# Optimization experiments

Measured on AMD Instinct MI355X. Metric: run time of the kernel, lower is better.

Reference implementation:

```python
import jax, jax.numpy as jnp
import numpy as np

BLOCK_SIZE = 32
NUM_PROJS = 7


def _unit_hamming(n):
    # AngularLSH._unit_hamming_distance_array (Gray-code-like permutation)
    a = np.array([0, 1], dtype=np.int32)
    for i in range(1, n):
        a = np.concatenate([a, a[::-1] + 2 ** i])
    return a


def _lsh_hash(x, proj_dir, perm, enc_vec):
    # x: [B,H,N,D], proj_dir: [1,1,D,P] -> hash ids [B,H,N]
    pd = proj_dir[0, 0]  # [D,P]
    proj = jnp.einsum('bhnd,dp->bhnp', x, pd)
    bits = (proj > 0).astype(jnp.int32)
    bin_ids = (bits * enc_vec).sum(-1)
    return perm[bin_ids]


def _causal_attn(q, k, v):
    # q,k,v: [B,N,H,D] (xformers layout), causal softmax attention
    B, N, H, D = q.shape
    s = jnp.einsum('bqhd,bkhd->bhqk', q, k) * (D ** -0.5)
    causal = jnp.tril(jnp.ones((N, N), dtype=bool))
    s = jnp.where(causal, s, jnp.finfo(s.dtype).min)
    w = jax.nn.softmax(s, axis=-1)
    return jnp.einsum('bhqk,bkhd->bqhd', w, v)


def _forward(q, k, v, proj_dir):
    B, N, H, D = q.shape
    bs = BLOCK_SIZE
    nb = N // bs
    perm = jnp.asarray(_unit_hamming(NUM_PROJS))
    enc_vec = jnp.asarray(2 ** np.arange(NUM_PROJS, dtype=np.int32))

    qt = jnp.transpose(q, (0, 2, 1, 3))  # [B,H,N,D]
    kt = jnp.transpose(k, (0, 2, 1, 3))

    q_hash = _lsh_hash(qt, proj_dir, perm, enc_vec)  # [B,H,N]
    sort_idx = jnp.argsort(q_hash, axis=2, stable=True)
    q_hash_sort = jnp.take_along_axis(q_hash, sort_idx, axis=2)
    inv_idx = jnp.argsort(sort_idx, axis=2, stable=True)
    q_sorted = jnp.take_along_axis(qt, sort_idx[..., None], axis=2)  # [B,H,N,D]

    k_hash = _lsh_hash(kt, proj_dir, perm, enc_vec)  # [B,H,N]

    # torch .view(seq_len, -1) on [B,H,N] contiguous tensors (C-order reshape)
    qh_rows = q_hash_sort.reshape(N, -1)  # [N, B*H]
    kh_rows = k_hash.reshape(N, -1)
    eq = (qh_rows == kh_rows).reshape(nb, -1)  # rows grouped by query block
    keep = (eq.sum(axis=1) > 0)  # [nb] block kept if any hash match

    # K_split_per_block = k.reshape(B, nb, -1, D) on [B,H,N,D]
    k_blocks = kt.reshape(B, nb, (H * N) // nb, D)
    k_blocks = k_blocks * keep[None, :, None, None].astype(kt.dtype)
    k_crit = k_blocks.reshape(B, H, N, D)

    # out_critical = attn(q_critical, k_critical, v_critical) then unsort
    out = _causal_attn(jnp.transpose(q_sorted, (0, 2, 1, 3)),
                       jnp.transpose(k_crit, (0, 2, 1, 3)),
                       v)  # [B,N,H,D]
    out = jnp.take_along_axis(jnp.transpose(out, (0, 2, 1, 3)), inv_idx[..., None], axis=2)
    return jnp.transpose(out, (0, 2, 1, 3))  # [B,N,H,D]


def setup_inputs() -> dict:
    key = jax.random.key(0)
    k1, k2, k3, k4 = jax.random.split(key, 4)
    B, N, H, D = 2, 2048, 16, 128
    return {
        'q': jax.random.normal(k1, (B, N, H, D), dtype=jnp.float32),
        'k': jax.random.normal(k2, (B, N, H, D), dtype=jnp.float32),
        'v': jax.random.normal(k3, (B, N, H, D), dtype=jnp.float32),
        'proj_dir': jax.random.normal(k4, (1, 1, D, NUM_PROJS), dtype=jnp.float32),
        'is_causal': 1,
        'mask': jnp.zeros((1, 1), dtype=bool),
    }


def reference(q, k, v, proj_dir, is_causal, mask):
    # is_causal is always True at every attention call site; mask is unused then.
    return _forward(q, k, v, proj_dir)
```

## Files before the change

### kernel.cpp

```cpp
#include <hip/hip_runtime.h>
#include <cstdint>

#define BB 2
#define NN 2048
#define HH 16
#define DD 128
#define BH 32
#define NPROJ 7

typedef __bf16 bf16x8 __attribute__((ext_vector_type(8)));
typedef float f32x4 __attribute__((ext_vector_type(4)));

__device__ __forceinline__ unsigned short f2bf(float f) {
  unsigned int u = __float_as_uint(f);
  u += 0x7fff + ((u >> 16) & 1);
  return (unsigned short)(u >> 16);
}

__device__ __forceinline__ bf16x8 load_q8(const float* p) {
  float4 a = *(const float4*)p;
  float4 b = *(const float4*)(p + 4);
  unsigned short r[8] = {f2bf(a.x), f2bf(a.y), f2bf(a.z), f2bf(a.w),
                         f2bf(b.x), f2bf(b.y), f2bf(b.z), f2bf(b.w)};
  return *(bf16x8*)r;
}

__global__ void prep_kernel(const float* __restrict__ q, const float* __restrict__ k,
                            const float* __restrict__ v, const float* __restrict__ pd,
                            int* __restrict__ qh, int* __restrict__ kh,
                            unsigned short* __restrict__ Vt, unsigned short* __restrict__ Kb) {
  __shared__ __align__(16) char smem[64 * 132 * 2];
  if (blockIdx.x < 4096) {
    float* spd = (float*)smem;
    for (int i = threadIdx.x; i < DD * NPROJ; i += 256) spd[i] = pd[i];
    __syncthreads();
    long long gid = (long long)blockIdx.x * 256 + threadIdx.x;
    int part = (int)(gid & 7);
    long long row = gid >> 3;
    const long long NR = (long long)BB * NN * HH;
    int isk = row >= NR;
    long long r = isk ? row - NR : row;
    const float* src = (isk ? k : q) + r * DD + part * 16;
    double acc[NPROJ];
    for (int p = 0; p < NPROJ; ++p) acc[p] = 0.0;
    __align__(16) unsigned short kb16[16];
    for (int d = 0; d < 16; d += 4) {
      float4 x = *(const float4*)(src + d);
      if (isk) {
        kb16[d + 0] = f2bf(x.x); kb16[d + 1] = f2bf(x.y);
        kb16[d + 2] = f2bf(x.z); kb16[d + 3] = f2bf(x.w);
      }
      int dbase = part * 16 + d;
      for (int p = 0; p < NPROJ; ++p) {
        acc[p] += (double)x.x * (double)spd[(dbase + 0) * NPROJ + p]
                + (double)x.y * (double)spd[(dbase + 1) * NPROJ + p]
                + (double)x.z * (double)spd[(dbase + 2) * NPROJ + p]
                + (double)x.w * (double)spd[(dbase + 3) * NPROJ + p];
      }
    }
    int b_ = (int)(r / (NN * HH));
    int rem = (int)(r % (NN * HH));
    int n_ = rem / HH, h_ = rem % HH;
    if (isk) {
      unsigned short* dst = Kb + (((long long)(b_ * HH + h_) * NN + n_) << 7) + part * 16;
      *(uint4*)dst = *(const uint4*)&kb16[0];
      *(uint4*)(dst + 8) = *(const uint4*)&kb16[8];
    }
    for (int off = 1; off < 8; off <<= 1)
      for (int p = 0; p < NPROJ; ++p) acc[p] += __shfl_xor(acc[p], off);
    if (part == 0) {
      int bin = 0;
      for (int p = 0; p < NPROJ; ++p) bin |= ((int)(acc[p] > 0.0)) << p;
      int hsh = bin ^ (bin >> 1);
      (isk ? kh : qh)[((long long)b_ * HH + h_) * NN + n_] = hsh;
    }
  } else {
    unsigned short (*tile)[132] = (unsigned short(*)[132])smem;
    int blk = blockIdx.x - 4096;
    int bh = blk >> 5;
    int n0 = (blk & 31) * 64;
    int b = bh >> 4, h = bh & 15;
    for (int it = 0; it < 8; ++it) {
      int cid = it * 256 + threadIdx.x;
      int r = cid >> 5, d4 = (cid & 31) * 4;
      float4 x = *(const float4*)(v + (((long long)(b * NN + n0 + r) * HH + h) << 7) + d4);
      *(ushort4*)&tile[r][d4] = make_ushort4(f2bf(x.x), f2bf(x.y), f2bf(x.z), f2bf(x.w));
    }
    __syncthreads();
    for (int it = 0; it < 8; ++it) {
      int cid = it * 256 + threadIdx.x;
      int d = cid >> 4, n4 = (cid & 15) * 4;
      ushort4 y = make_ushort4(tile[n4 + 0][d], tile[n4 + 1][d], tile[n4 + 2][d], tile[n4 + 3][d]);
      *(ushort4*)(Vt + ((long long)bh * DD + d) * NN + n0 + n4) = y;
    }
  }
}

__global__ void sortkeep_kernel(const int* __restrict__ qh, const int* __restrict__ kh,
                                int* __restrict__ sidx, int* __restrict__ keep) {
  __shared__ int sh[NN];
  __shared__ int cnt[4][128];
  __shared__ int cum[128];
  __shared__ int kflag[2];
  int bh = blockIdx.x;
  const int* src = qh + (long long)bh * NN;
  for (int i = threadIdx.x; i < NN; i += 512) sh[i] = src[i];
  if (threadIdx.x < 2) kflag[threadIdx.x] = 0;
  __syncthreads();
  int bin = threadIdx.x & 127, seg = threadIdx.x >> 7;
  int n0 = seg * (NN / 4);
  int c = 0;
  for (int n = n0; n < n0 + NN / 4; ++n) c += (sh[n] == bin);
  cnt[seg][bin] = c;
  __syncthreads();
  if (threadIdx.x == 0) {
    int run = 0;
    for (int t = 0; t < 128; ++t) {
      cum[t] = run;
      run += cnt[0][t] + cnt[1][t] + cnt[2][t] + cnt[3][t];
    }
  }
  __syncthreads();
  int pos = cum[bin];
  for (int s = 0; s < seg; ++s) pos += cnt[s][bin];
  int f0 = 0, f1 = 0;
  for (int n = n0; n < n0 + NN / 4; ++n)
    if (sh[n] == bin) {
      sidx[(long long)bh * NN + pos] = n;
      int match = (bin == kh[(long long)bh * NN + pos]);
      if (pos < 1024) f0 |= match; else f1 |= match;
      ++pos;
    }
  if (f0) atomicOr(&kflag[0], 1);
  if (f1) atomicOr(&kflag[1], 1);
  __syncthreads();
  if (threadIdx.x < 2) keep[bh * 2 + threadIdx.x] = kflag[threadIdx.x];
}

__global__ __launch_bounds__(256, 2)
void flash_kernel(const float* __restrict__ q, const unsigned short* __restrict__ Kb,
                  const unsigned short* __restrict__ Vt, const int* __restrict__ sidx,
                  const int* __restrict__ keep, float* __restrict__ out) {
  __shared__ __align__(16) unsigned short Kt[2][64 * 136];
  __shared__ __align__(16) unsigned short Vs[2][128 * 72];
  __shared__ __align__(16) unsigned short Pb[4][16 * 72];

  int bx = blockIdx.x;
  int bh = blockIdx.y;
  int b = bh >> 4, h = bh & 15;
  int tid = threadIdx.x;
  int w = tid >> 6, lane = tid & 63;
  int l16 = lane & 15, qd = lane >> 4;

  const unsigned short* Kh = Kb + (long long)bh * NN * DD;
  const unsigned short* Vb = Vt + (long long)bh * DD * NN;
  const float scale = 0.088388347648318447f;

  const int ksr = tid >> 4;
  const int ksc = (tid & 15) * 8;
  const int vsr = tid >> 3;
  const int vsc = (tid & 7) * 8;

  uint4 kreg[4], vreg[4];

#define STAGE_LOAD(K0, KP)                                                            \
  {                                                                                   \
    if (KP) {                                                                         \
      _Pragma("unroll")                                                               \
      for (int it = 0; it < 4; ++it)                                                  \
        kreg[it] = *(const uint4*)(Kh + (long long)((K0) + it * 16 + ksr) * DD + ksc);\
    } else {                                                                          \
      _Pragma("unroll")                                                               \
      for (int it = 0; it < 4; ++it) kreg[it] = make_uint4(0, 0, 0, 0);               \
    }                                                                                 \
    _Pragma("unroll")                                                                 \
    for (int it = 0; it < 4; ++it)                                                    \
      vreg[it] = *(const uint4*)(Vb + (long long)(it * 32 + vsr) * NN + (K0) + vsc);  \
  }

#define STAGE_WRITE(BUF)                                                              \
  {                                                                                   \
    _Pragma("unroll")                                                                 \
    for (int it = 0; it < 4; ++it)                                                    \
      *(uint4*)&Kt[BUF][(it * 16 + ksr) * 136 + ksc] = kreg[it];                      \
    _Pragma("unroll")                                                                 \
    for (int it = 0; it < 4; ++it)                                                    \
      *(uint4*)&Vs[BUF][(it * 32 + vsr) * 72 + vsc] = vreg[it];                       \
  }

  for (int ph = 0; ph < 2; ++ph) {
    int qt = ph ? bx : 31 - bx;
    int qrow = qt * 64 + w * 16 + l16;

    bf16x8 qf[4];
    {
      int nq = sidx[bh * NN + qrow];
      const float* p0 = q + (((long long)(b * NN + nq) * HH + h) << 7) + qd * 8;
#pragma unroll
      for (int c = 0; c < 4; ++c) qf[c] = load_q8(p0 + c * 32);
    }
    f32x4 o[8];
#pragma unroll
    for (int i = 0; i < 8; ++i) o[i] = (f32x4){0.f, 0.f, 0.f, 0.f};
    float m = -__builtin_inff(), l = 0.f;

    int cur = 0;
    STAGE_LOAD(0, keep[h * 4]);
    __syncthreads();
    STAGE_WRITE(0);
    __syncthreads();

    for (int kb = 0; kb <= qt; ++kb) {
      if (kb < qt) STAGE_LOAD((kb + 1) * 64, keep[h * 4 + ((kb + 1) >> 3)]);

      int k0 = kb * 64;
      const unsigned short* Ktc = Kt[cur];
      const unsigned short* Vsc = Vs[cur];

      float s[16];
#pragma unroll
      for (int t = 0; t < 4; ++t) {
        f32x4 a1 = (f32x4){0.f, 0.f, 0.f, 0.f};
#pragma unroll
        for (int c = 0; c < 4; ++c) {
          bf16x8 kf = *(const bf16x8*)&Ktc[(t * 16 + l16) * 136 + c * 32 + qd * 8];
          a1 = __builtin_amdgcn_mfma_f32_16x16x32_bf16(kf, qf[c], a1, 0, 0, 0);
        }
        if (kb == qt) {
#pragma unroll
          for (int r = 0; r < 4; ++r) {
            int keyg = k0 + t * 16 + qd * 4 + r;
            s[t * 4 + r] = (keyg > qrow) ? -__builtin_inff() : a1[r] * scale;
          }
        } else {
#pragma unroll
          for (int r = 0; r < 4; ++r) s[t * 4 + r] = a1[r] * scale;
        }
      }

      {
        float mloc = s[0];
#pragma unroll
        for (int i = 1; i < 16; ++i) mloc = fmaxf(mloc, s[i]);
        mloc = fmaxf(mloc, __shfl_xor(mloc, 16));
        mloc = fmaxf(mloc, __shfl_xor(mloc, 32));
        if (__any(mloc > m)) {
          float mnew = fmaxf(m, mloc);
          float alpha = __expf(m - mnew);
          float aO[4];
#pragma unroll
          for (int r = 0; r < 4; ++r) aO[r] = __shfl(alpha, qd * 4 + r);
#pragma unroll
          for (int c8 = 0; c8 < 8; ++c8)
#pragma unroll
            for (int r = 0; r < 4; ++r) o[c8][r] *= aO[r];
          l *= alpha;
          m = mnew;
        }
        float psum = 0.f;
#pragma unroll
        for (int t = 0; t < 4; ++t) {
          float p0 = __expf(s[t * 4 + 0] - m);
          float p1 = __expf(s[t * 4 + 1] - m);
          float p2 = __expf(s[t * 4 + 2] - m);
          float p3 = __expf(s[t * 4 + 3] - m);
          psum += (p0 + p1) + (p2 + p3);
          *(ushort4*)&Pb[w][l16 * 72 + t * 16 + qd * 4] =
              make_ushort4(f2bf(p0), f2bf(p1), f2bf(p2), f2bf(p3));
        }
        psum += __shfl_xor(psum, 16);
        psum += __shfl_xor(psum, 32);
        l += psum;
      }

#pragma unroll
      for (int g = 0; g < 2; ++g) {
        bf16x8 pf = *(const bf16x8*)&Pb[w][l16 * 72 + g * 32 + qd * 8];
#pragma unroll
        for (int c8 = 0; c8 < 8; ++c8) {
          bf16x8 vf = *(const bf16x8*)&Vsc[(c8 * 16 + l16) * 72 + g * 32 + qd * 8];
          o[c8] = __builtin_amdgcn_mfma_f32_16x16x32_bf16(pf, vf, o[c8], 0, 0, 0);
        }
      }

      if (kb < qt) {
        STAGE_WRITE(cur ^ 1);
        __syncthreads();
        cur ^= 1;
      }
    }

    float lO[4];
    int nO[4];
#pragma unroll
    for (int r = 0; r < 4; ++r) {
      lO[r] = __shfl(l, qd * 4 + r);
      nO[r] = sidx[(long long)bh * NN + qt * 64 + w * 16 + qd * 4 + r];
    }
#pragma unroll
    for (int r = 0; r < 4; ++r) {
      float inv = 1.f / lO[r];
      float* ob = out + (((long long)(b * NN + nO[r]) * HH + h) << 7) + l16;
#pragma unroll
      for (int c8 = 0; c8 < 8; ++c8)
        ob[c8 * 16] = o[c8][r] * inv;
    }
  }
#undef STAGE_LOAD
#undef STAGE_WRITE
}

extern "C" void kernel_launch(void* const* d_in, const int* in_sizes, int n_in,
                              void* d_out, int out_size, void* d_ws, size_t ws_size,
                              hipStream_t stream) {
  const float* q = (const float*)d_in[0];
  const float* k = (const float*)d_in[1];
  const float* v = (const float*)d_in[2];
  const float* pd = (const float*)d_in[3];
  float* out = (float*)d_out;
  char* ws = (char*)d_ws;
  int* qh   = (int*)(ws + 0);
  int* kh   = (int*)(ws + (1u << 18));
  int* sidx = (int*)(ws + (2u << 18));
  int* keep = (int*)(ws + 3u * (1u << 18));
  unsigned short* Vt = (unsigned short*)(ws + (2u << 20));
  unsigned short* Kb = (unsigned short*)(ws + (18u << 20));

  prep_kernel<<<5120, 256, 0, stream>>>(q, k, v, pd, qh, kh, Vt, Kb);
  sortkeep_kernel<<<32, 512, 0, stream>>>(qh, kh, sidx, keep);
  flash_kernel<<<dim3(16, 32), 256, 0, stream>>>(q, Kb, Vt, sidx, keep, out);
}
```

Before: 359.5 us.

## Process two 16-row query groups per wave to double K/V tile reuse

Each wave now computes two 16-row query groups against each staged K/V tile, making the query tile 128 rows per block and halving the grid. This amortizes LDS staging, K fragment loads and V fragment loads over twice the MFMA work. In exchange the kernel holds twice the accumulators and drops to one block per CU, reducing occupancy and latency hiding.

```diff
diff --git a/kernel.cpp b/kernel.cpp
--- a/kernel.cpp
+++ b/kernel.cpp
@@ -137,13 +137,13 @@
   if (threadIdx.x < 2) keep[bh * 2 + threadIdx.x] = kflag[threadIdx.x];
 }
 
-__global__ __launch_bounds__(256, 2)
+__global__ __launch_bounds__(256, 1)
 void flash_kernel(const float* __restrict__ q, const unsigned short* __restrict__ Kb,
                   const unsigned short* __restrict__ Vt, const int* __restrict__ sidx,
                   const int* __restrict__ keep, float* __restrict__ out) {
   __shared__ __align__(16) unsigned short Kt[2][64 * 136];
   __shared__ __align__(16) unsigned short Vs[2][128 * 72];
-  __shared__ __align__(16) unsigned short Pb[4][16 * 72];
+  __shared__ __align__(16) unsigned short Pb[4][32 * 72];
 
   int bx = blockIdx.x;
   int bh = blockIdx.y;
@@ -189,20 +189,32 @@
   }
 
   for (int ph = 0; ph < 2; ++ph) {
-    int qt = ph ? bx : 31 - bx;
-    int qrow = qt * 64 + w * 16 + l16;
-
-    bf16x8 qf[4];
+    int QT = ph ? bx : 15 - bx;
+    int qrowA = QT * 128 + w * 32 + l16;
+    int qrowB = qrowA + 16;
+
+    bf16x8 qfA[4], qfB[4];
     {
-      int nq = sidx[bh * NN + qrow];
-      const float* p0 = q + (((long long)(b * NN + nq) * HH + h) << 7) + qd * 8;
-#pragma unroll
-      for (int c = 0; c < 4; ++c) qf[c] = load_q8(p0 + c * 32);
-    }
-    f32x4 o[8];
-#pragma unroll
-    for (int i = 0; i < 8; ++i) o[i] = (f32x4){0.f, 0.f, 0.f, 0.f};
-    float m = -__builtin_inff(), l = 0.f;
+      int nqA = sidx[bh * NN + qrowA];
+      int nqB = sidx[bh * NN + qrowB];
+      const float* pA = q + (((long long)(b * NN + nqA) * HH + h) << 7) + qd * 8;
+      const float* pB = q + (((long long)(b * NN + nqB) * HH + h) << 7) + qd * 8;
+#pragma unroll
+      for (int c = 0; c < 4; ++c) {
+        qfA[c] = load_q8(pA + c * 32);
+        qfB[c] = load_q8(pB + c * 32);
+      }
+    }
+    f32x4 oA[8], oB[8];
+#pragma unroll
+    for (int i = 0; i < 8; ++i) {
+      oA[i] = (f32x4){0.f, 0.f, 0.f, 0.f};
+      oB[i] = (f32x4){0.f, 0.f, 0.f, 0.f};
+    }
+    float mA = -__builtin_inff(), lA = 0.f;
+    float mB = -__builtin_inff(), lB = 0.f;
+
+    int NKB = 2 * QT + 2;
 
     int cur = 0;
     STAGE_LOAD(0, keep[h * 4]);
@@ -210,100 +222,146 @@
     STAGE_WRITE(0);
     __syncthreads();
 
-    for (int kb = 0; kb <= qt; ++kb) {
-      if (kb < qt) STAGE_LOAD((kb + 1) * 64, keep[h * 4 + ((kb + 1) >> 3)]);
+    for (int kb = 0; kb < NKB; ++kb) {
+      if (kb + 1 < NKB) STAGE_LOAD((kb + 1) * 64, keep[h * 4 + ((kb + 1) >> 3)]);
 
       int k0 = kb * 64;
       const unsigned short* Ktc = Kt[cur];
       const unsigned short* Vsc = Vs[cur];
 
-      float s[16];
+      float sA[16], sB[16];
 #pragma unroll
       for (int t = 0; t < 4; ++t) {
-        f32x4 a1 = (f32x4){0.f, 0.f, 0.f, 0.f};
+        f32x4 aA = (f32x4){0.f, 0.f, 0.f, 0.f};
+        f32x4 aB = (f32x4){0.f, 0.f, 0.f, 0.f};
 #pragma unroll
         for (int c = 0; c < 4; ++c) {
           bf16x8 kf = *(const bf16x8*)&Ktc[(t * 16 + l16) * 136 + c * 32 + qd * 8];
-          a1 = __builtin_amdgcn_mfma_f32_16x16x32_bf16(kf, qf[c], a1, 0, 0, 0);
-        }
-        if (kb == qt) {
+          aA = __builtin_amdgcn_mfma_f32_16x16x32_bf16(kf, qfA[c], aA, 0, 0, 0);
+          aB = __builtin_amdgcn_mfma_f32_16x16x32_bf16(kf, qfB[c], aB, 0, 0, 0);
+        }
+        if (kb >= 2 * QT) {
 #pragma unroll
           for (int r = 0; r < 4; ++r) {
             int keyg = k0 + t * 16 + qd * 4 + r;
-            s[t * 4 + r] = (keyg > qrow) ? -__builtin_inff() : a1[r] * scale;
+            sA[t * 4 + r] = (keyg > qrowA) ? -__builtin_inff() : aA[r] * scale;
+            sB[t * 4 + r] = (keyg > qrowB) ? -__builtin_inff() : aB[r] * scale;
           }
         } else {
 #pragma unroll
-          for (int r = 0; r < 4; ++r) s[t * 4 + r] = a1[r] * scale;
+          for (int r = 0; r < 4; ++r) {
+            sA[t * 4 + r] = aA[r] * scale;
+            sB[t * 4 + r] = aB[r] * scale;
+          }
         }
       }
 
       {
-        float mloc = s[0];
-#pragma unroll
-        for (int i = 1; i < 16; ++i) mloc = fmaxf(mloc, s[i]);
+        float mloc = sA[0];
+#pragma unroll
+        for (int i = 1; i < 16; ++i) mloc = fmaxf(mloc, sA[i]);
         mloc = fmaxf(mloc, __shfl_xor(mloc, 16));
         mloc = fmaxf(mloc, __shfl_xor(mloc, 32));
-        if (__any(mloc > m)) {
-          float mnew = fmaxf(m, mloc);
-          float alpha = __expf(m - mnew);
+        if (__any(mloc > mA)) {
+          float mnew = fmaxf(mA, mloc);
+          float alpha = __expf(mA - mnew);
           float aO[4];
 #pragma unroll
           for (int r = 0; r < 4; ++r) aO[r] = __shfl(alpha, qd * 4 + r);
 #pragma unroll
           for (int c8 = 0; c8 < 8; ++c8)
 #pragma unroll
-            for (int r = 0; r < 4; ++r) o[c8][r] *= aO[r];
-          l *= alpha;
-          m = mnew;
+            for (int r = 0; r < 4; ++r) oA[c8][r] *= aO[r];
+          lA *= alpha;
+          mA = mnew;
         }
         float psum = 0.f;
 #pragma unroll
         for (int t = 0; t < 4; ++t) {
-          float p0 = __expf(s[t * 4 + 0] - m);
-          float p1 = __expf(s[t * 4 + 1] - m);
-          float p2 = __expf(s[t * 4 + 2] - m);
-          float p3 = __expf(s[t * 4 + 3] - m);
+          float p0 = __expf(sA[t * 4 + 0] - mA);
+          float p1 = __expf(sA[t * 4 + 1] - mA);
+          float p2 = __expf(sA[t * 4 + 2] - mA);
+          float p3 = __expf(sA[t * 4 + 3] - mA);
           psum += (p0 + p1) + (p2 + p3);
           *(ushort4*)&Pb[w][l16 * 72 + t * 16 + qd * 4] =
               make_ushort4(f2bf(p0), f2bf(p1), f2bf(p2), f2bf(p3));
         }
         psum += __shfl_xor(psum, 16);
         psum += __shfl_xor(psum, 32);
-        l += psum;
+        lA += psum;
+      }
+      {
+        float mloc = sB[0];
+#pragma unroll
+        for (int i = 1; i < 16; ++i) mloc = fmaxf(mloc, sB[i]);
+        mloc = fmaxf(mloc, __shfl_xor(mloc, 16));
+        mloc = fmaxf(mloc, __shfl_xor(mloc, 32));
+        if (__any(mloc > mB)) {
+          float mnew = fmaxf(mB, mloc);
+          float alpha = __expf(mB - mnew);
+          float aO[4];
+#pragma unroll
+          for (int r = 0; r < 4; ++r) aO[r] = __shfl(alpha, qd * 4 + r);
+#pragma unroll
+          for (int c8 = 0; c8 < 8; ++c8)
+#pragma unroll
+            for (int r = 0; r < 4; ++r) oB[c8][r] *= aO[r];
+          lB *= alpha;
+          mB = mnew;
+        }
+        float psum = 0.f;
+#pragma unroll
+        for (int t = 0; t < 4; ++t) {
+          float p0 = __expf(sB[t * 4 + 0] - mB);
+          float p1 = __expf(sB[t * 4 + 1] - mB);
+          float p2 = __expf(sB[t * 4 + 2] - mB);
+          float p3 = __expf(sB[t * 4 + 3] - mB);
+          psum += (p0 + p1) + (p2 + p3);
+          *(ushort4*)&Pb[w][(16 + l16) * 72 + t * 16 + qd * 4] =
+              make_ushort4(f2bf(p0), f2bf(p1), f2bf(p2), f2bf(p3));
+        }
+        psum += __shfl_xor(psum, 16);
+        psum += __shfl_xor(psum, 32);
+        lB += psum;
       }
 
 #pragma unroll
       for (int g = 0; g < 2; ++g) {
-        bf16x8 pf = *(const bf16x8*)&Pb[w][l16 * 72 + g * 32 + qd * 8];
+        bf16x8 pfA = *(const bf16x8*)&Pb[w][l16 * 72 + g * 32 + qd * 8];
+        bf16x8 pfB = *(const bf16x8*)&Pb[w][(16 + l16) * 72 + g * 32 + qd * 8];
 #pragma unroll
         for (int c8 = 0; c8 < 8; ++c8) {
           bf16x8 vf = *(const bf16x8*)&Vsc[(c8 * 16 + l16) * 72 + g * 32 + qd * 8];
-          o[c8] = __builtin_amdgcn_mfma_f32_16x16x32_bf16(pf, vf, o[c8], 0, 0, 0);
-        }
-      }
-
-      if (kb < qt) {
+          oA[c8] = __builtin_amdgcn_mfma_f32_16x16x32_bf16(pfA, vf, oA[c8], 0, 0, 0);
+          oB[c8] = __builtin_amdgcn_mfma_f32_16x16x32_bf16(pfB, vf, oB[c8], 0, 0, 0);
+        }
+      }
+
+      if (kb + 1 < NKB) {
         STAGE_WRITE(cur ^ 1);
         __syncthreads();
         cur ^= 1;
       }
     }
 
-    float lO[4];
-    int nO[4];
-#pragma unroll
-    for (int r = 0; r < 4; ++r) {
-      lO[r] = __shfl(l, qd * 4 + r);
-      nO[r] = sidx[(long long)bh * NN + qt * 64 + w * 16 + qd * 4 + r];
-    }
-#pragma unroll
-    for (int r = 0; r < 4; ++r) {
-      float inv = 1.f / lO[r];
-      float* ob = out + (((long long)(b * NN + nO[r]) * HH + h) << 7) + l16;
-#pragma unroll
-      for (int c8 = 0; c8 < 8; ++c8)
-        ob[c8 * 16] = o[c8][r] * inv;
+#pragma unroll
+    for (int grp = 0; grp < 2; ++grp) {
+      float lg = grp ? lB : lA;
+      float lO[4];
+      int nO[4];
+#pragma unroll
+      for (int r = 0; r < 4; ++r) {
+        lO[r] = __shfl(lg, qd * 4 + r);
+        nO[r] = sidx[(long long)bh * NN + QT * 128 + w * 32 + grp * 16 + qd * 4 + r];
+      }
+#pragma unroll
+      for (int r = 0; r < 4; ++r) {
+        float inv = 1.f / lO[r];
+        float* ob = out + (((long long)(b * NN + nO[r]) * HH + h) << 7) + l16;
+#pragma unroll
+        for (int c8 = 0; c8 < 8; ++c8)
+          ob[c8 * 16] = (grp ? oB : oA)[c8][r] * inv;
+      }
     }
   }
 #undef STAGE_LOAD
@@ -328,5 +386,5 @@
 
   prep_kernel<<<5120, 256, 0, stream>>>(q, k, v, pd, qh, kh, Vt, Kb);
   sortkeep_kernel<<<32, 512, 0, stream>>>(qh, kh, sidx, keep);
-  flash_kernel<<<dim3(16, 32), 256, 0, stream>>>(q, Kb, Vt, sidx, keep, out);
-}
+  flash_kernel<<<dim3(8, 32), 256, 0, stream>>>(q, Kb, Vt, sidx, keep, out);
+}
```

Result: slower. 371.5 us (+3.3%).

## Software-pipeline QK of next tile with softmax and PV of current tile

Applied to the files above, without the earlier changes.

Restructures the attention inner loop so the QK^T MFMAs for key tile kb+1 are issued between the softmax of tile kb and its PV accumulation, with two score buffers alternated by manual unrolling. Global prefetch now runs two tiles ahead, and LDS staging gets barriers on both sides. The intent is to overlap matrix-core work with the exp/max/shuffle softmax latency. In exchange it holds more registers (two score arrays), which may cut occupancy, and adds an extra barrier per step.

```diff
diff --git a/kernel.cpp b/kernel.cpp
--- a/kernel.cpp
+++ b/kernel.cpp
@@ -188,6 +188,97 @@
       *(uint4*)&Vs[BUF][(it * 32 + vsr) * 72 + vsc] = vreg[it];                       \
   }
 
+#define QK_TILE(T, S)                                                                 \
+  {                                                                                   \
+    const unsigned short* Ktc_ = Kt[(T) & 1];                                         \
+    int k0_ = (T) * 64;                                                               \
+    _Pragma("unroll")                                                                 \
+    for (int t = 0; t < 4; ++t) {                                                     \
+      f32x4 a1 = (f32x4){0.f, 0.f, 0.f, 0.f};                                         \
+      _Pragma("unroll")                                                               \
+      for (int c = 0; c < 4; ++c) {                                                   \
+        bf16x8 kf = *(const bf16x8*)&Ktc_[(t * 16 + l16) * 136 + c * 32 + qd * 8];    \
+        a1 = __builtin_amdgcn_mfma_f32_16x16x32_bf16(kf, qf[c], a1, 0, 0, 0);         \
+      }                                                                               \
+      if ((T) == qt) {                                                                \
+        _Pragma("unroll")                                                             \
+        for (int r = 0; r < 4; ++r) {                                                 \
+          int keyg = k0_ + t * 16 + qd * 4 + r;                                       \
+          (S)[t * 4 + r] = (keyg > qrow) ? -__builtin_inff() : a1[r] * scale;         \
+        }                                                                             \
+      } else {                                                                        \
+        _Pragma("unroll")                                                             \
+        for (int r = 0; r < 4; ++r) (S)[t * 4 + r] = a1[r] * scale;                   \
+      }                                                                               \
+    }                                                                                 \
+  }
+
+#define SOFTMAX_UPDATE(S)                                                             \
+  {                                                                                   \
+    float x0_ = fmaxf(fmaxf((S)[0], (S)[1]), fmaxf((S)[2], (S)[3]));                  \
+    float x1_ = fmaxf(fmaxf((S)[4], (S)[5]), fmaxf((S)[6], (S)[7]));                  \
+    float x2_ = fmaxf(fmaxf((S)[8], (S)[9]), fmaxf((S)[10], (S)[11]));                \
+    float x3_ = fmaxf(fmaxf((S)[12], (S)[13]), fmaxf((S)[14], (S)[15]));              \
+    float mloc = fmaxf(fmaxf(x0_, x1_), fmaxf(x2_, x3_));                             \
+    mloc = fmaxf(mloc, __shfl_xor(mloc, 16));                                         \
+    mloc = fmaxf(mloc, __shfl_xor(mloc, 32));                                         \
+    if (__any(mloc > m)) {                         \
+      float mnew = fmaxf(m, mloc);                                                    \
+      float alpha = __expf(m - mnew);                                                 \
+      float aO[4];                                                                    \
+      _Pragma("unroll")                                                               \
+      for (int r = 0; r < 4; ++r) aO[r] = __shfl(alpha, qd * 4 + r);                  \
+      _Pragma("unroll")                                                               \
+      for (int c8 = 0; c8 < 8; ++c8)                                                  \
+        _Pragma("unroll")                                                             \
+        for (int r = 0; r < 4; ++r) o[c8][r] *= aO[r];                                \
+      l *= alpha;                                                                     \
+      m = mnew;                                                                       \
+    }                                                                                 \
+    float psum = 0.f;                                                                 \
+    _Pragma("unroll")                                                                 \
+    for (int t = 0; t < 4; ++t) {                                                     \
+      float p0 = __expf((S)[t * 4 + 0] - m);                                          \
+      float p1 = __expf((S)[t * 4 + 1] - m);                                          \
+      float p2 = __expf((S)[t * 4 + 2] - m);                                          \
+      float p3 = __expf((S)[t * 4 + 3] - m);                                          \
+      psum += (p0 + p1) + (p2 + p3);                                                  \
+      *(ushort4*)&Pb[w][l16 * 72 + t * 16 + qd * 4] =                                 \
+          make_ushort4(f2bf(p0), f2bf(p1), f2bf(p2), f2bf(p3));                       \
+    }                                                                                 \
+    psum += __shfl_xor(psum, 16);                                                     \
+    psum += __shfl_xor(psum, 32);                                                     \
+    l += psum;                                                                        \
+  }
+
+#define PV_ACC(BUF)                                                                   \
+  {                                                                                   \
+    const unsigned short* Vsc_ = Vs[BUF];                                             \
+    _Pragma("unroll")                                                                 \
+    for (int g = 0; g < 2; ++g) {                                                     \
+      bf16x8 pf = *(const bf16x8*)&Pb[w][l16 * 72 + g * 32 + qd * 8];                 \
+      _Pragma("unroll")                                                               \
+      for (int c8 = 0; c8 < 8; ++c8) {                                                \
+        bf16x8 vf = *(const bf16x8*)&Vsc_[(c8 * 16 + l16) * 72 + g * 32 + qd * 8];    \
+        o[c8] = __builtin_amdgcn_mfma_f32_16x16x32_bf16(pf, vf, o[c8], 0, 0, 0);      \
+      }                                                                               \
+    }                                                                                 \
+  }
+
+#define STEP(KB, SC, SN)                                                              \
+  {                                                                                   \
+    int nxt_ = (KB) + 1;                                                              \
+    if (nxt_ <= qt) {                                                                 \
+      __syncthreads();                       \
+      STAGE_WRITE(nxt_ & 1);                                                          \
+      __syncthreads();                               \
+      if (nxt_ + 1 <= qt) STAGE_LOAD((nxt_ + 1) * 64, keep[h * 4 + ((nxt_ + 1) >> 3)]); \
+    }                                                                                 \
+    SOFTMAX_UPDATE(SC);                                                               \
+    if (nxt_ <= qt) QK_TILE(nxt_, SN);                                                \
+    PV_ACC((KB) & 1);                                                                 \
+  }
+
   for (int ph = 0; ph < 2; ++ph) {
     int qt = ph ? bx : 31 - bx;
     int qrow = qt * 64 + w * 16 + l16;
@@ -204,90 +295,19 @@
     for (int i = 0; i < 8; ++i) o[i] = (f32x4){0.f, 0.f, 0.f, 0.f};
     float m = -__builtin_inff(), l = 0.f;
 
-    int cur = 0;
     STAGE_LOAD(0, keep[h * 4]);
     __syncthreads();
     STAGE_WRITE(0);
     __syncthreads();
-
-    for (int kb = 0; kb <= qt; ++kb) {
-      if (kb < qt) STAGE_LOAD((kb + 1) * 64, keep[h * 4 + ((kb + 1) >> 3)]);
-
-      int k0 = kb * 64;
-      const unsigned short* Ktc = Kt[cur];
-      const unsigned short* Vsc = Vs[cur];
-
-      float s[16];
-#pragma unroll
-      for (int t = 0; t < 4; ++t) {
-        f32x4 a1 = (f32x4){0.f, 0.f, 0.f, 0.f};
-#pragma unroll
-        for (int c = 0; c < 4; ++c) {
-          bf16x8 kf = *(const bf16x8*)&Ktc[(t * 16 + l16) * 136 + c * 32 + qd * 8];
-          a1 = __builtin_amdgcn_mfma_f32_16x16x32_bf16(kf, qf[c], a1, 0, 0, 0);
-        }
-        if (kb == qt) {
-#pragma unroll
-          for (int r = 0; r < 4; ++r) {
-            int keyg = k0 + t * 16 + qd * 4 + r;
-            s[t * 4 + r] = (keyg > qrow) ? -__builtin_inff() : a1[r] * scale;
-          }
-        } else {
-#pragma unroll
-          for (int r = 0; r < 4; ++r) s[t * 4 + r] = a1[r] * scale;
-        }
-      }
-
-      {
-        float mloc = s[0];
-#pragma unroll
-        for (int i = 1; i < 16; ++i) mloc = fmaxf(mloc, s[i]);
-        mloc = fmaxf(mloc, __shfl_xor(mloc, 16));
-        mloc = fmaxf(mloc, __shfl_xor(mloc, 32));
-        if (__any(mloc > m)) {
-          float mnew = fmaxf(m, mloc);
-          float alpha = __expf(m - mnew);
-          float aO[4];
-#pragma unroll
-          for (int r = 0; r < 4; ++r) aO[r] = __shfl(alpha, qd * 4 + r);
-#pragma unroll
-          for (int c8 = 0; c8 < 8; ++c8)
-#pragma unroll
-            for (int r = 0; r < 4; ++r) o[c8][r] *= aO[r];
-          l *= alpha;
-          m = mnew;
-        }
-        float psum = 0.f;
-#pragma unroll
-        for (int t = 0; t < 4; ++t) {
-          float p0 = __expf(s[t * 4 + 0] - m);
-          float p1 = __expf(s[t * 4 + 1] - m);
-          float p2 = __expf(s[t * 4 + 2] - m);
-          float p3 = __expf(s[t * 4 + 3] - m);
-          psum += (p0 + p1) + (p2 + p3);
-          *(ushort4*)&Pb[w][l16 * 72 + t * 16 + qd * 4] =
-              make_ushort4(f2bf(p0), f2bf(p1), f2bf(p2), f2bf(p3));
-        }
-        psum += __shfl_xor(psum, 16);
-        psum += __shfl_xor(psum, 32);
-        l += psum;
-      }
-
-#pragma unroll
-      for (int g = 0; g < 2; ++g) {
-        bf16x8 pf = *(const bf16x8*)&Pb[w][l16 * 72 + g * 32 + qd * 8];
-#pragma unroll
-        for (int c8 = 0; c8 < 8; ++c8) {
-          bf16x8 vf = *(const bf16x8*)&Vsc[(c8 * 16 + l16) * 72 + g * 32 + qd * 8];
-          o[c8] = __builtin_amdgcn_mfma_f32_16x16x32_bf16(pf, vf, o[c8], 0, 0, 0);
-        }
-      }
-
-      if (kb < qt) {
-        STAGE_WRITE(cur ^ 1);
-        __syncthreads();
-        cur ^= 1;
-      }
+    if (qt > 0) STAGE_LOAD(64, keep[h * 4]);
+
+    float s0[16], s1[16];
+    QK_TILE(0, s0);
+
+    int kb = 0;
+    while (true) {
+      STEP(kb, s0, s1); ++kb; if (kb > qt) break;
+      STEP(kb, s1, s0); ++kb; if (kb > qt) break;
     }
 
     float lO[4];
@@ -306,6 +326,10 @@
         ob[c8 * 16] = o[c8][r] * inv;
     }
   }
+#undef STEP
+#undef PV_ACC
+#undef SOFTMAX_UPDATE
+#undef QK_TILE
 #undef STAGE_LOAD
 #undef STAGE_WRITE
 }
```

New measurement: 366.1 us. No clear change (+1.8%).

## Split paired causal query tiles into separate blocks with single-buffered LDS

Applied to the files above, without the earlier changes.

The flash kernel previously paired a heavy and a light causal query tile in each block across 16x32 blocks. It now launches one query tile per block (32x32 grid), ordered longest-first, and drops double-buffered K/V shared memory to a single buffer with an extra barrier, raising the occupancy hint to 3 blocks per SM. It also adds s_setprio around the MFMA sections and uses a tree max reduction. The intent is more parallelism and occupancy, at the cost of less load/compute overlap per block and dependence on the hardware scheduler for balancing the uneven tile lengths.

```diff
diff --git a/kernel.cpp b/kernel.cpp
--- a/kernel.cpp
+++ b/kernel.cpp
@@ -137,16 +137,16 @@
   if (threadIdx.x < 2) keep[bh * 2 + threadIdx.x] = kflag[threadIdx.x];
 }
 
-__global__ __launch_bounds__(256, 2)
+__global__ __launch_bounds__(256, 3)
 void flash_kernel(const float* __restrict__ q, const unsigned short* __restrict__ Kb,
                   const unsigned short* __restrict__ Vt, const int* __restrict__ sidx,
                   const int* __restrict__ keep, float* __restrict__ out) {
-  __shared__ __align__(16) unsigned short Kt[2][64 * 136];
-  __shared__ __align__(16) unsigned short Vs[2][128 * 72];
+  __shared__ __align__(16) unsigned short Kt[64 * 136];
+  __shared__ __align__(16) unsigned short Vs[128 * 72];
   __shared__ __align__(16) unsigned short Pb[4][16 * 72];
 
-  int bx = blockIdx.x;
-  int bh = blockIdx.y;
+  int bh = blockIdx.x;
+  int qt = 31 - (int)blockIdx.y;
   int b = bh >> 4, h = bh & 15;
   int tid = threadIdx.x;
   int w = tid >> 6, lane = tid & 63;
@@ -178,133 +178,132 @@
       vreg[it] = *(const uint4*)(Vb + (long long)(it * 32 + vsr) * NN + (K0) + vsc);  \
   }
 
-#define STAGE_WRITE(BUF)                                                              \
+#define STAGE_WRITE()                                                                 \
   {                                                                                   \
     _Pragma("unroll")                                                                 \
     for (int it = 0; it < 4; ++it)                                                    \
-      *(uint4*)&Kt[BUF][(it * 16 + ksr) * 136 + ksc] = kreg[it];                      \
+      *(uint4*)&Kt[(it * 16 + ksr) * 136 + ksc] = kreg[it];                           \
     _Pragma("unroll")                                                                 \
     for (int it = 0; it < 4; ++it)                                                    \
-      *(uint4*)&Vs[BUF][(it * 32 + vsr) * 72 + vsc] = vreg[it];                       \
-  }
-
-  for (int ph = 0; ph < 2; ++ph) {
-    int qt = ph ? bx : 31 - bx;
-    int qrow = qt * 64 + w * 16 + l16;
-
-    bf16x8 qf[4];
+      *(uint4*)&Vs[(it * 32 + vsr) * 72 + vsc] = vreg[it];                            \
+  }
+
+  int qrow = qt * 64 + w * 16 + l16;
+
+  bf16x8 qf[4];
+  {
+    int nq = sidx[bh * NN + qrow];
+    const float* p0 = q + (((long long)(b * NN + nq) * HH + h) << 7) + qd * 8;
+#pragma unroll
+    for (int c = 0; c < 4; ++c) qf[c] = load_q8(p0 + c * 32);
+  }
+  f32x4 o[8];
+#pragma unroll
+  for (int i = 0; i < 8; ++i) o[i] = (f32x4){0.f, 0.f, 0.f, 0.f};
+  float m = -__builtin_inff(), l = 0.f;
+
+  STAGE_LOAD(0, keep[h * 4]);
+  STAGE_WRITE();
+  __syncthreads();
+
+  for (int kb = 0; kb <= qt; ++kb) {
+    if (kb < qt) STAGE_LOAD((kb + 1) * 64, keep[h * 4 + ((kb + 1) >> 3)]);
+
+    int k0 = kb * 64;
+
+    float s[16];
+    __builtin_amdgcn_s_setprio(1);
+#pragma unroll
+    for (int t = 0; t < 4; ++t) {
+      f32x4 a1 = (f32x4){0.f, 0.f, 0.f, 0.f};
+#pragma unroll
+      for (int c = 0; c < 4; ++c) {
+        bf16x8 kf = *(const bf16x8*)&Kt[(t * 16 + l16) * 136 + c * 32 + qd * 8];
+        a1 = __builtin_amdgcn_mfma_f32_16x16x32_bf16(kf, qf[c], a1, 0, 0, 0);
+      }
+      if (kb == qt) {
+#pragma unroll
+        for (int r = 0; r < 4; ++r) {
+          int keyg = k0 + t * 16 + qd * 4 + r;
+          s[t * 4 + r] = (keyg > qrow) ? -__builtin_inff() : a1[r] * scale;
+        }
+      } else {
+#pragma unroll
+        for (int r = 0; r < 4; ++r) s[t * 4 + r] = a1[r] * scale;
+      }
+    }
+    __builtin_amdgcn_s_setprio(0);
+
     {
-      int nq = sidx[bh * NN + qrow];
-      const float* p0 = q + (((long long)(b * NN + nq) * HH + h) << 7) + qd * 8;
-#pragma unroll
-      for (int c = 0; c < 4; ++c) qf[c] = load_q8(p0 + c * 32);
-    }
-    f32x4 o[8];
-#pragma unroll
-    for (int i = 0; i < 8; ++i) o[i] = (f32x4){0.f, 0.f, 0.f, 0.f};
-    float m = -__builtin_inff(), l = 0.f;
-
-    int cur = 0;
-    STAGE_LOAD(0, keep[h * 4]);
-    __syncthreads();
-    STAGE_WRITE(0);
-    __syncthreads();
-
-    for (int kb = 0; kb <= qt; ++kb) {
-      if (kb < qt) STAGE_LOAD((kb + 1) * 64, keep[h * 4 + ((kb + 1) >> 3)]);
-
-      int k0 = kb * 64;
-      const unsigned short* Ktc = Kt[cur];
-      const unsigned short* Vsc = Vs[cur];
-
-      float s[16];
+      float x0 = fmaxf(fmaxf(s[0], s[1]), fmaxf(s[2], s[3]));
+      float x1 = fmaxf(fmaxf(s[4], s[5]), fmaxf(s[6], s[7]));
+      float x2 = fmaxf(fmaxf(s[8], s[9]), fmaxf(s[10], s[11]));
+      float x3 = fmaxf(fmaxf(s[12], s[13]), fmaxf(s[14], s[15]));
+      float mloc = fmaxf(fmaxf(x0, x1), fmaxf(x2, x3));
+      mloc = fmaxf(mloc, __shfl_xor(mloc, 16));
+      mloc = fmaxf(mloc, __shfl_xor(mloc, 32));
+      if (__any(mloc > m)) {
+        float mnew = fmaxf(m, mloc);
+        float alpha = __expf(m - mnew);
+        float aO[4];
+#pragma unroll
+        for (int r = 0; r < 4; ++r) aO[r] = __shfl(alpha, qd * 4 + r);
+#pragma unroll
+        for (int c8 = 0; c8 < 8; ++c8)
+#pragma unroll
+          for (int r = 0; r < 4; ++r) o[c8][r] *= aO[r];
+        l *= alpha;
+        m = mnew;
+      }
+      float psum = 0.f;
 #pragma unroll
       for (int t = 0; t < 4; ++t) {
-        f32x4 a1 = (f32x4){0.f, 0.f, 0.f, 0.f};
-#pragma unroll
-        for (int c = 0; c < 4; ++c) {
-          bf16x8 kf = *(const bf16x8*)&Ktc[(t * 16 + l16) * 136 + c * 32 + qd * 8];
-          a1 = __builtin_amdgcn_mfma_f32_16x16x32_bf16(kf, qf[c], a1, 0, 0, 0);
-        }
-        if (kb == qt) {
-#pragma unroll
-          for (int r = 0; r < 4; ++r) {
-            int keyg = k0 + t * 16 + qd * 4 + r;
-            s[t * 4 + r] = (keyg > qrow) ? -__builtin_inff() : a1[r] * scale;
-          }
-        } else {
-#pragma unroll
-          for (int r = 0; r < 4; ++r) s[t * 4 + r] = a1[r] * scale;
-        }
-      }
-
-      {
-        float mloc = s[0];
-#pragma unroll
-        for (int i = 1; i < 16; ++i) mloc = fmaxf(mloc, s[i]);
-        mloc = fmaxf(mloc, __shfl_xor(mloc, 16));
-        mloc = fmaxf(mloc, __shfl_xor(mloc, 32));
-        if (__any(mloc > m)) {
-          float mnew = fmaxf(m, mloc);
-          float alpha = __expf(m - mnew);
-          float aO[4];
-#pragma unroll
-          for (int r = 0; r < 4; ++r) aO[r] = __shfl(alpha, qd * 4 + r);
-#pragma unroll
-          for (int c8 = 0; c8 < 8; ++c8)
-#pragma unroll
-            for (int r = 0; r < 4; ++r) o[c8][r] *= aO[r];
-          l *= alpha;
-          m = mnew;
-        }
-        float psum = 0.f;
-#pragma unroll
-        for (int t = 0; t < 4; ++t) {
-          float p0 = __expf(s[t * 4 + 0] - m);
-          float p1 = __expf(s[t * 4 + 1] - m);
-          float p2 = __expf(s[t * 4 + 2] - m);
-          float p3 = __expf(s[t * 4 + 3] - m);
-          psum += (p0 + p1) + (p2 + p3);
-          *(ushort4*)&Pb[w][l16 * 72 + t * 16 + qd * 4] =
-              make_ushort4(f2bf(p0), f2bf(p1), f2bf(p2), f2bf(p3));
-        }
-        psum += __shfl_xor(psum, 16);
-        psum += __shfl_xor(psum, 32);
-        l += psum;
-      }
-
-#pragma unroll
-      for (int g = 0; g < 2; ++g) {
-        bf16x8 pf = *(const bf16x8*)&Pb[w][l16 * 72 + g * 32 + qd * 8];
-#pragma unroll
-        for (int c8 = 0; c8 < 8; ++c8) {
-          bf16x8 vf = *(const bf16x8*)&Vsc[(c8 * 16 + l16) * 72 + g * 32 + qd * 8];
-          o[c8] = __builtin_amdgcn_mfma_f32_16x16x32_bf16(pf, vf, o[c8], 0, 0, 0);
-        }
-      }
-
-      if (kb < qt) {
-        STAGE_WRITE(cur ^ 1);
-        __syncthreads();
-        cur ^= 1;
-      }
-    }
-
-    float lO[4];
-    int nO[4];
-#pragma unroll
-    for (int r = 0; r < 4; ++r) {
-      lO[r] = __shfl(l, qd * 4 + r);
-      nO[r] = sidx[(long long)bh * NN + qt * 64 + w * 16 + qd * 4 + r];
-    }
-#pragma unroll
-    for (int r = 0; r < 4; ++r) {
-      float inv = 1.f / lO[r];
-      float* ob = out + (((long long)(b * NN + nO[r]) * HH + h) << 7) + l16;
-#pragma unroll
-      for (int c8 = 0; c8 < 8; ++c8)
-        ob[c8 * 16] = o[c8][r] * inv;
-    }
+        float p0 = __expf(s[t * 4 + 0] - m);
+        float p1 = __expf(s[t * 4 + 1] - m);
+        float p2 = __expf(s[t * 4 + 2] - m);
+        float p3 = __expf(s[t * 4 + 3] - m);
+        psum += (p0 + p1) + (p2 + p3);
+        *(ushort4*)&Pb[w][l16 * 72 + t * 16 + qd * 4] =
+            make_ushort4(f2bf(p0), f2bf(p1), f2bf(p2), f2bf(p3));
+      }
+      psum += __shfl_xor(psum, 16);
+      psum += __shfl_xor(psum, 32);
+      l += psum;
+    }
+
+    __builtin_amdgcn_s_setprio(1);
+#pragma unroll
+    for (int g = 0; g < 2; ++g) {
+      bf16x8 pf = *(const bf16x8*)&Pb[w][l16 * 72 + g * 32 + qd * 8];
+#pragma unroll
+      for (int c8 = 0; c8 < 8; ++c8) {
+        bf16x8 vf = *(const bf16x8*)&Vs[(c8 * 16 + l16) * 72 + g * 32 + qd * 8];
+        o[c8] = __builtin_amdgcn_mfma_f32_16x16x32_bf16(pf, vf, o[c8], 0, 0, 0);
+      }
+    }
+    __builtin_amdgcn_s_setprio(0);
+
+    if (kb < qt) {
+      __syncthreads();
+      STAGE_WRITE();
+      __syncthreads();
+    }
+  }
+
+  float lO[4];
+  int nO[4];
+#pragma unroll
+  for (int r = 0; r < 4; ++r) {
+    lO[r] = __shfl(l, qd * 4 + r);
+    nO[r] = sidx[(long long)bh * NN + qt * 64 + w * 16 + qd * 4 + r];
+  }
+#pragma unroll
+  for (int r = 0; r < 4; ++r) {
+    float inv = 1.f / lO[r];
+    float* ob = out + (((long long)(b * NN + nO[r]) * HH + h) << 7) + l16;
+#pragma unroll
+    for (int c8 = 0; c8 < 8; ++c8)
+      ob[c8 * 16] = o[c8][r] * inv;
   }
 #undef STAGE_LOAD
 #undef STAGE_WRITE
@@ -328,5 +327,5 @@
 
   prep_kernel<<<5120, 256, 0, stream>>>(q, k, v, pd, qh, kh, Vt, Kb);
   sortkeep_kernel<<<32, 512, 0, stream>>>(qh, kh, sidx, keep);
-  flash_kernel<<<dim3(16, 32), 256, 0, stream>>>(q, Kb, Vt, sidx, keep, out);
-}
+  flash_kernel<<<dim3(32, 32), 256, 0, stream>>>(q, Kb, Vt, sidx, keep, out);
+}
```

After: 344.1 us. -4.3%, faster.
